# Kernel tuning notes

Measured on AMD Instinct MI355X. Metric: run time of the kernel, lower is better.

The kernel has to match this reference:

```python
import jax, jax.numpy as jnp
import numpy as np
from jax import lax

B, C, N, T = 8, 512, 256, 32  # batch, channels (c_in==c_out), nodes, timesteps


def setup_inputs() -> dict:
    key = jax.random.key(0)
    ks = jax.random.split(key, 5)
    x = jax.random.normal(ks[0], (B, C, N, T), dtype=jnp.float32)
    # 8 Line_Transforms: w1,w3,w5,w7 act on input x (gates i,f,o,g); w2,w4,w6,w8 act on h.
    # torch.rand init -> uniform [0,1). Weights (c_out,c_in), bias (c_in,1)==(C,1).
    Wx = jax.random.uniform(ks[1], (4, C, C), dtype=jnp.float32)
    bx = jax.random.uniform(ks[2], (4, C, 1), dtype=jnp.float32)
    Wh = jax.random.uniform(ks[3], (4, C, C), dtype=jnp.float32)
    bh = jax.random.uniform(ks[4], (4, C, 1), dtype=jnp.float32)
    return {"x": x, "Wx": Wx, "bx": bx, "Wh": Wh, "bh": bh}


def reference(x, Wx, bx, Wh, bh):
    b, f, n, t = x.shape
    c = Wx.shape[1]
    # Precompute all input-side gate projections for every timestep in one big GEMM.
    # xp: (T, 4, B, C, N); bias (4,C,1) broadcasts over batch and nodes.
    xp = jnp.einsum('gcf,bfnt->tgbcn', Wx, x) + bx[None, :, None]

    h0 = jnp.zeros((b, c, n), dtype=x.dtype)
    c0 = jnp.zeros((b, c, n), dtype=x.dtype)

    def step(carry, xp_t):
        h, cell = carry
        # hidden-side projections for all 4 gates at once: (4, B, C, N)
        hp = jnp.einsum('gcf,bfn->gbcn', Wh, h) + bh[:, None]
        z = xp_t + hp
        i = jax.nn.sigmoid(z[0])
        fg = jax.nn.sigmoid(z[1])
        o = jax.nn.sigmoid(z[2])
        g = jnp.tanh(z[3])
        new_c = fg * cell + i * g
        new_h = o * jnp.tanh(new_c)
        return (new_h, new_c), new_h

    _, hs = lax.scan(step, (h0, c0), xp)  # hs: (T, B, C, N)
    return jnp.moveaxis(hs, 0, -1)  # (B, C, N, T)
```

## Files before the change

### kernel.cpp

```cpp
#include <hip/hip_runtime.h>
#include <hip/hip_bf16.h>
#include <stdint.h>

typedef _Float16 f16x8 __attribute__((ext_vector_type(8)));
typedef float f32x16 __attribute__((ext_vector_type(16)));

#define MFMA __builtin_amdgcn_mfma_f32_32x32x16_f16

#define XP_OFF   0ull
#define HP_OFF   134217728ull
#define WT_OFF   142606336ull
#define BI_OFF   150994944ull
#define CS_OFF   151257088ull
#define HT_OFF   155451392ull

__device__ __forceinline__ void gload16(const void* g, void* s) {
    __builtin_amdgcn_global_load_lds((const __attribute__((address_space(1))) void*)g,
                                     (__attribute__((address_space(3))) void*)s, 16, 0, 0);
}

__global__ __launch_bounds__(256) void init_kernel(
    const float* __restrict__ Wx, const float* __restrict__ Wh,
    const float* __restrict__ bx, const float* __restrict__ bh, char* __restrict__ ws)
{
    f16x8* Wt = (f16x8*)(ws + WT_OFF);
    float* bi = (float*)(ws + BI_OFF);
    float4* cs = (float4*)(ws + CS_OFF);
    uint4* hp0 = (uint4*)(ws + HP_OFF);
    int tid = blockIdx.x * 256 + threadIdx.x;
    int stride = gridDim.x * 256;
    for (int i = tid; i < 262144; i += stride) {
        int l = i & 63, ks = (i >> 6) & 1, nt = (i >> 7) & 3, kk = (i >> 9) & 31, nblk = i >> 14;
        int n = nblk * 128 + nt * 32 + (l & 31);
        int k = kk * 32 + ks * 16 + 8 * (l >> 5);
        int c = n >> 2, g = n & 3;
        const float* src = (k < 512) ? (Wx + ((size_t)(g * 512 + c)) * 512 + k)
                                     : (Wh + ((size_t)(g * 512 + c)) * 512 + (k - 512));
        f16x8 hi, lo;
#pragma unroll
        for (int e = 0; e < 8; ++e) {
            float v = src[e];
            _Float16 h = (_Float16)v;
            hi[e] = h; lo[e] = (_Float16)(v - (float)h);
        }
        size_t base = (size_t)((i >> 6) * 2) * 64 + (i & 63);
        Wt[base] = hi;
        Wt[base + 64] = lo;
    }
    for (int i = tid; i < 65536; i += stride) {
        int r = i & 15, l = (i >> 4) & 63, nt = (i >> 10) & 3, nblk = i >> 12;
        int n = nblk * 128 + nt * 32 + (r & 3) + 8 * (r >> 2) + 4 * (l >> 5);
        int c = n >> 2, g = n & 3;
        bi[i] = bx[g * 512 + c] + bh[g * 512 + c];
    }
    for (int i = tid; i < 262144; i += stride) cs[i] = make_float4(0.f, 0.f, 0.f, 0.f);
    for (int i = tid; i < 262144; i += stride) hp0[i] = make_uint4(0u, 0u, 0u, 0u);
}

__global__ __launch_bounds__(256) void xpose_kernel(const float* __restrict__ x, f16x8* __restrict__ xp)
{
    __shared__ float tile[8448];
    int tid = threadIdx.x;
    int jblk = blockIdx.x, jt = blockIdx.y, fq = blockIdx.z;
    int jbase = jblk * 128 + jt * 32;
    for (int fg = 0; fg < 16; ++fg) {
        int fgg = fq * 16 + fg;
        {
            int jl = tid & 31, fo = tid >> 5;
            int j = jbase + jl, b = j >> 8, n = j & 255, f = fgg * 8 + fo;
            const float4* src = (const float4*)(x + (((size_t)(b * 512 + f)) * 256 + n) * 32);
            float* dst = &tile[(fo * 32 + jl) * 33];
#pragma unroll
            for (int i2 = 0; i2 < 8; ++i2) {
                float4 v = src[i2];
                dst[4 * i2 + 0] = v.x; dst[4 * i2 + 1] = v.y;
                dst[4 * i2 + 2] = v.z; dst[4 * i2 + 3] = v.w;
            }
        }
        __syncthreads();
        {
            int jl = tid & 31, tq = tid >> 5;
            int kk = fgg >> 2, ks = (fgg >> 1) & 1, hb = fgg & 1;
            int l = hb * 32 + jl;
#pragma unroll
            for (int ti = 0; ti < 4; ++ti) {
                int t = tq * 4 + ti;
                f16x8 hi, lo;
#pragma unroll
                for (int e = 0; e < 8; ++e) {
                    float v = tile[(e * 32 + jl) * 33 + t];
                    _Float16 h = (_Float16)v;
                    hi[e] = h; lo[e] = (_Float16)(v - (float)h);
                }
                size_t base = ((((size_t)t * 16 + jblk) * 16 + kk) * 4 + jt) * 4 + ks * 2;
                xp[(base + 0) * 64 + l] = hi;
                xp[(base + 1) * 64 + l] = lo;
            }
        }
        __syncthreads();
    }
}

__global__ __launch_bounds__(256, 1) void step_kernel(
    const f16x8* __restrict__ xp_t,
    const f16x8* __restrict__ hp_in,
    f16x8* __restrict__ hp_out,
    const f16x8* __restrict__ Wt,
    const float4* __restrict__ bi4,
    float4* __restrict__ cst4,
    _Float16* __restrict__ hsTt)
{
    __shared__ f16x8 actl[2][1024];
    const int tid = threadIdx.x;
    const int l = tid & 63;
    const int w = tid >> 6;
    const int wn = w >> 1, wj = w & 1;
    const int bid = blockIdx.x;
    const int idx = bid >> 3;
    const int nblk = ((bid & 7) << 1) | (idx & 1);
    const int jblk = idx >> 1;
    const int nt0 = wn * 2, jt0 = wj * 2;

    f32x16 acc00 = {0.f,0.f,0.f,0.f,0.f,0.f,0.f,0.f,0.f,0.f,0.f,0.f,0.f,0.f,0.f,0.f};
    f32x16 acc01 = acc00, acc10 = acc00, acc11 = acc00;
    f16x8 wtc0, wtc1, wtc2, wtc3, wtc4, wtc5, wtc6, wtc7;
    f16x8 wtn0, wtn1, wtn2, wtn3, wtn4, wtn5, wtn6, wtn7;

#define STAGE(bi_, kkv) do { \
    const f16x8* asrc = ((kkv) < 16) ? (xp_t + (size_t)(jblk * 16 + (kkv)) * 1024) \
                                     : (hp_in + (size_t)(jblk * 16 + ((kkv) - 16)) * 1024); \
    gload16(asrc + tid,       &actl[bi_][tid]); \
    gload16(asrc + tid + 256, &actl[bi_][tid + 256]); \
    gload16(asrc + tid + 512, &actl[bi_][tid + 512]); \
    gload16(asrc + tid + 768, &actl[bi_][tid + 768]); \
} while (0)

#define LOADW(P, kkv) do { \
    size_t wb = (size_t)((nblk * 32 + (kkv)) * 16 + nt0 * 4) * 64 + l; \
    P##0 = Wt[wb + 0 * 64]; P##1 = Wt[wb + 1 * 64]; P##2 = Wt[wb + 2 * 64]; P##3 = Wt[wb + 3 * 64]; \
    P##4 = Wt[wb + 4 * 64]; P##5 = Wt[wb + 5 * 64]; P##6 = Wt[wb + 6 * 64]; P##7 = Wt[wb + 7 * 64]; \
} while (0)

#define COMP_KS(bi_, whi0, wlo0, whi1, wlo1, ksv) do { \
    int ab = ((jt0 * 2 + (ksv)) * 2) * 64 + l; \
    f16x8 ahi0 = actl[bi_][ab], alo0 = actl[bi_][ab + 64]; \
    f16x8 ahi1 = actl[bi_][ab + 256], alo1 = actl[bi_][ab + 320]; \
    acc00 = MFMA(whi0, ahi0, acc00, 0, 0, 0); \
    acc00 = MFMA(wlo0, ahi0, acc00, 0, 0, 0); \
    acc00 = MFMA(whi0, alo0, acc00, 0, 0, 0); \
    acc01 = MFMA(whi0, ahi1, acc01, 0, 0, 0); \
    acc01 = MFMA(wlo0, ahi1, acc01, 0, 0, 0); \
    acc01 = MFMA(whi0, alo1, acc01, 0, 0, 0); \
    acc10 = MFMA(whi1, ahi0, acc10, 0, 0, 0); \
    acc10 = MFMA(wlo1, ahi0, acc10, 0, 0, 0); \
    acc10 = MFMA(whi1, alo0, acc10, 0, 0, 0); \
    acc11 = MFMA(whi1, ahi1, acc11, 0, 0, 0); \
    acc11 = MFMA(wlo1, ahi1, acc11, 0, 0, 0); \
    acc11 = MFMA(whi1, alo1, acc11, 0, 0, 0); \
} while (0)

#define COMPUTE(bi_, P) do { \
    COMP_KS(bi_, P##0, P##1, P##4, P##5, 0); \
    COMP_KS(bi_, P##2, P##3, P##6, P##7, 1); \
} while (0)

    STAGE(0, 0); LOADW(wtc, 0);
    __syncthreads();
    for (int kk2 = 0; kk2 < 16; ++kk2) {
        const int kkA = kk2 * 2;
        STAGE(1, kkA + 1); LOADW(wtn, kkA + 1);
        COMPUTE(0, wtc);
        __syncthreads();
        if (kk2 < 15) { STAGE(0, kkA + 2); LOADW(wtc, kkA + 2); }
        COMPUTE(1, wtn);
        __syncthreads();
    }

    const int p = l >> 5;
#define GATE(accV, q, bq, coldc, cnoutc, hqv) do { \
    float zi = accV[4 * (q) + 0] + bq.x; \
    float zf = accV[4 * (q) + 1] + bq.y; \
    float zo = accV[4 * (q) + 2] + bq.z; \
    float zg = accV[4 * (q) + 3] + bq.w; \
    float ig = 1.f / (1.f + expf(-zi)); \
    float fg = 1.f / (1.f + expf(-zf)); \
    float og = 1.f / (1.f + expf(-zo)); \
    float gg = tanhf(zg); \
    float cn = fg * coldc + ig * gg; \
    cnoutc = cn; \
    hqv = og * tanhf(cn); \
} while (0)

#define EPI(accV, ntl, jtl) do { \
    int nt = nt0 + (ntl), jt = jt0 + (jtl); \
    size_t bb = ((size_t)(nblk * 4 + nt) * 64 + l) * 4; \
    float4 bq0 = bi4[bb + 0], bq1 = bi4[bb + 1], bq2 = bi4[bb + 2], bq3 = bi4[bb + 3]; \
    size_t ci = (((size_t)(jblk * 16 + nblk) * 4 + jt) * 4 + nt) * 64 + l; \
    float4 cold = cst4[ci]; \
    float4 cnew; \
    float hq0, hq1, hq2, hq3; \
    GATE(accV, 0, bq0, cold.x, cnew.x, hq0); \
    GATE(accV, 1, bq1, cold.y, cnew.y, hq1); \
    GATE(accV, 2, bq2, cold.z, cnew.z, hq2); \
    GATE(accV, 3, bq3, cold.w, cnew.w, hq3); \
    cst4[ci] = cnew; \
    float hr0 = __shfl_xor(hq0, 32); \
    float hr1 = __shfl_xor(hq1, 32); \
    float hr2 = __shfl_xor(hq2, 32); \
    float hr3 = __shfl_xor(hq3, 32); \
    float e0 = p ? hr0 : hq0, e1 = p ? hq0 : hr0; \
    float e2 = p ? hr1 : hq1, e3 = p ? hq1 : hr1; \
    float e4 = p ? hr2 : hq2, e5 = p ? hq2 : hr2; \
    float e6 = p ? hr3 : hq3, e7 = p ? hq3 : hr3; \
    f16x8 hhi, hlo; \
    hhi[0] = (_Float16)e0; hhi[1] = (_Float16)e1; hhi[2] = (_Float16)e2; hhi[3] = (_Float16)e3; \
    hhi[4] = (_Float16)e4; hhi[5] = (_Float16)e5; hhi[6] = (_Float16)e6; hhi[7] = (_Float16)e7; \
    hlo[0] = (_Float16)(e0 - (float)hhi[0]); hlo[1] = (_Float16)(e1 - (float)hhi[1]); \
    hlo[2] = (_Float16)(e2 - (float)hhi[2]); hlo[3] = (_Float16)(e3 - (float)hhi[3]); \
    hlo[4] = (_Float16)(e4 - (float)hhi[4]); hlo[5] = (_Float16)(e5 - (float)hhi[5]); \
    hlo[6] = (_Float16)(e6 - (float)hhi[6]); hlo[7] = (_Float16)(e7 - (float)hhi[7]); \
    if (p == (nt & 1)) { \
        size_t hb = ((((size_t)(jblk * 16 + nblk) * 4 + jt) * 2 + (nt >> 1))) * 2; \
        hp_out[(hb + 0) * 64 + l] = hhi; \
        hp_out[(hb + 1) * 64 + l] = hlo; \
        int j = jblk * 128 + jt * 32 + (l & 31); \
        int c0 = nblk * 32 + nt * 8; \
        *(f16x8*)(hsTt + (size_t)j * 512 + c0) = hhi; \
    } \
} while (0)

    EPI(acc00, 0, 0);
    EPI(acc01, 0, 1);
    EPI(acc10, 1, 0);
    EPI(acc11, 1, 1);
}

__global__ __launch_bounds__(256) void oxpose_kernel(
    const _Float16* __restrict__ hsT, float* __restrict__ out)
{
    int tid = threadIdx.x;
    int bidx = blockIdx.x;
    int c = ((bidx & 1) << 8) + tid;
    int bn = bidx >> 1;
    int b = bn >> 8, n = bn & 255;
    float vals[32];
#pragma unroll
    for (int t = 0; t < 32; ++t)
        vals[t] = (float)hsT[((size_t)t * 2048 + bn) * 512 + c];
    float4* dst = (float4*)(out + (((size_t)(b * 512 + c)) * 256 + n) * 32);
#pragma unroll
    for (int i = 0; i < 8; ++i) {
        float4 v;
        v.x = vals[4 * i + 0]; v.y = vals[4 * i + 1];
        v.z = vals[4 * i + 2]; v.w = vals[4 * i + 3];
        dst[i] = v;
    }
}

extern "C" void kernel_launch(void* const* d_in, const int* in_sizes, int n_in,
                              void* d_out, int out_size, void* d_ws, size_t ws_size,
                              hipStream_t stream)
{
    const float* x  = (const float*)d_in[0];
    const float* Wx = (const float*)d_in[1];
    const float* bx = (const float*)d_in[2];
    const float* Wh = (const float*)d_in[3];
    const float* bh = (const float*)d_in[4];
    float* out = (float*)d_out;

    char* ws = (char*)d_ws;
    f16x8*  xp   = (f16x8*)(ws + XP_OFF);
    f16x8*  hp   = (f16x8*)(ws + HP_OFF);
    f16x8*  Wt   = (f16x8*)(ws + WT_OFF);
    float4* bi4  = (float4*)(ws + BI_OFF);
    float4* cst4 = (float4*)(ws + CS_OFF);
    _Float16* hsT = (_Float16*)(ws + HT_OFF);

    init_kernel<<<2048, 256, 0, stream>>>(Wx, Wh, bx, bh, ws);
    xpose_kernel<<<dim3(16, 4, 4), 256, 0, stream>>>(x, xp);
    for (int t = 0; t < 32; ++t) {
        step_kernel<<<256, 256, 0, stream>>>(
            xp + (size_t)t * 262144,
            hp + (size_t)(t & 1) * 262144,
            hp + (size_t)((t + 1) & 1) * 262144,
            Wt, bi4, cst4,
            hsT + (size_t)t * 2048 * 512);
    }
    oxpose_kernel<<<4096, 256, 0, stream>>>(hsT, out);
}
```

Measured before the change: 1.533 ms.

## Halve per-block step tile to double grid; flatten xpose loop across grid

The step kernel now gives each wave one n-tile instead of two, so each block computes half the output and the grid grows from 256 to 512 blocks. Launch bounds allow two blocks per CU, and per-wave weight registers and accumulators are halved. The xpose kernel drops its inner 16-iteration loop and launches 64 z-blocks instead of 4, which gives the transpose more parallelism. The cost is that each activation tile staged in LDS is reused by fewer MFMAs, so activation loads from global memory double.

```diff
diff --git a/kernel.cpp b/kernel.cpp
--- a/kernel.cpp
+++ b/kernel.cpp
@@ -61,47 +61,43 @@
 {
     __shared__ float tile[8448];
     int tid = threadIdx.x;
-    int jblk = blockIdx.x, jt = blockIdx.y, fq = blockIdx.z;
+    int jblk = blockIdx.x, jt = blockIdx.y, fgg = blockIdx.z;
     int jbase = jblk * 128 + jt * 32;
-    for (int fg = 0; fg < 16; ++fg) {
-        int fgg = fq * 16 + fg;
-        {
-            int jl = tid & 31, fo = tid >> 5;
-            int j = jbase + jl, b = j >> 8, n = j & 255, f = fgg * 8 + fo;
-            const float4* src = (const float4*)(x + (((size_t)(b * 512 + f)) * 256 + n) * 32);
-            float* dst = &tile[(fo * 32 + jl) * 33];
-#pragma unroll
-            for (int i2 = 0; i2 < 8; ++i2) {
-                float4 v = src[i2];
-                dst[4 * i2 + 0] = v.x; dst[4 * i2 + 1] = v.y;
-                dst[4 * i2 + 2] = v.z; dst[4 * i2 + 3] = v.w;
+    {
+        int jl = tid & 31, fo = tid >> 5;
+        int j = jbase + jl, b = j >> 8, n = j & 255, f = fgg * 8 + fo;
+        const float4* src = (const float4*)(x + (((size_t)(b * 512 + f)) * 256 + n) * 32);
+        float* dst = &tile[(fo * 32 + jl) * 33];
+#pragma unroll
+        for (int i2 = 0; i2 < 8; ++i2) {
+            float4 v = src[i2];
+            dst[4 * i2 + 0] = v.x; dst[4 * i2 + 1] = v.y;
+            dst[4 * i2 + 2] = v.z; dst[4 * i2 + 3] = v.w;
+        }
+    }
+    __syncthreads();
+    {
+        int jl = tid & 31, tq = tid >> 5;
+        int kk = fgg >> 2, ks = (fgg >> 1) & 1, hb = fgg & 1;
+        int l = hb * 32 + jl;
+#pragma unroll
+        for (int ti = 0; ti < 4; ++ti) {
+            int t = tq * 4 + ti;
+            f16x8 hi, lo;
+#pragma unroll
+            for (int e = 0; e < 8; ++e) {
+                float v = tile[(e * 32 + jl) * 33 + t];
+                _Float16 h = (_Float16)v;
+                hi[e] = h; lo[e] = (_Float16)(v - (float)h);
             }
+            size_t base = ((((size_t)t * 16 + jblk) * 16 + kk) * 4 + jt) * 4 + ks * 2;
+            xp[(base + 0) * 64 + l] = hi;
+            xp[(base + 1) * 64 + l] = lo;
         }
-        __syncthreads();
-        {
-            int jl = tid & 31, tq = tid >> 5;
-            int kk = fgg >> 2, ks = (fgg >> 1) & 1, hb = fgg & 1;
-            int l = hb * 32 + jl;
-#pragma unroll
-            for (int ti = 0; ti < 4; ++ti) {
-                int t = tq * 4 + ti;
-                f16x8 hi, lo;
-#pragma unroll
-                for (int e = 0; e < 8; ++e) {
-                    float v = tile[(e * 32 + jl) * 33 + t];
-                    _Float16 h = (_Float16)v;
-                    hi[e] = h; lo[e] = (_Float16)(v - (float)h);
-                }
-                size_t base = ((((size_t)t * 16 + jblk) * 16 + kk) * 4 + jt) * 4 + ks * 2;
-                xp[(base + 0) * 64 + l] = hi;
-                xp[(base + 1) * 64 + l] = lo;
-            }
-        }
-        __syncthreads();
-    }
-}
-
-__global__ __launch_bounds__(256, 1) void step_kernel(
+    }
+}
+
+__global__ __launch_bounds__(256, 2) void step_kernel(
     const f16x8* __restrict__ xp_t,
     const f16x8* __restrict__ hp_in,
     f16x8* __restrict__ hp_out,
@@ -117,14 +113,16 @@
     const int wn = w >> 1, wj = w & 1;
     const int bid = blockIdx.x;
     const int idx = bid >> 3;
-    const int nblk = ((bid & 7) << 1) | (idx & 1);
-    const int jblk = idx >> 1;
-    const int nt0 = wn * 2, jt0 = wj * 2;
-
-    f32x16 acc00 = {0.f,0.f,0.f,0.f,0.f,0.f,0.f,0.f,0.f,0.f,0.f,0.f,0.f,0.f,0.f,0.f};
-    f32x16 acc01 = acc00, acc10 = acc00, acc11 = acc00;
-    f16x8 wtc0, wtc1, wtc2, wtc3, wtc4, wtc5, wtc6, wtc7;
-    f16x8 wtn0, wtn1, wtn2, wtn3, wtn4, wtn5, wtn6, wtn7;
+    const int nblk4 = ((bid & 7) << 2) | (idx & 3);
+    const int jblk = idx >> 2;
+    const int nblk = nblk4 >> 1;
+    const int nt = ((nblk4 & 1) << 1) | wn;
+    const int jt0 = wj * 2;
+
+    f32x16 acc0 = {0.f,0.f,0.f,0.f,0.f,0.f,0.f,0.f,0.f,0.f,0.f,0.f,0.f,0.f,0.f,0.f};
+    f32x16 acc1 = acc0;
+    f16x8 wtc0, wtc1, wtc2, wtc3;
+    f16x8 wtn0, wtn1, wtn2, wtn3;
 
 #define STAGE(bi_, kkv) do { \
     const f16x8* asrc = ((kkv) < 16) ? (xp_t + (size_t)(jblk * 16 + (kkv)) * 1024) \
@@ -136,32 +134,26 @@
 } while (0)
 
 #define LOADW(P, kkv) do { \
-    size_t wb = (size_t)((nblk * 32 + (kkv)) * 16 + nt0 * 4) * 64 + l; \
-    P##0 = Wt[wb + 0 * 64]; P##1 = Wt[wb + 1 * 64]; P##2 = Wt[wb + 2 * 64]; P##3 = Wt[wb + 3 * 64]; \
-    P##4 = Wt[wb + 4 * 64]; P##5 = Wt[wb + 5 * 64]; P##6 = Wt[wb + 6 * 64]; P##7 = Wt[wb + 7 * 64]; \
-} while (0)
-
-#define COMP_KS(bi_, whi0, wlo0, whi1, wlo1, ksv) do { \
+    size_t wb = (size_t)((nblk * 32 + (kkv)) * 16 + nt * 4) * 64 + l; \
+    P##0 = Wt[wb + 0 * 64]; P##1 = Wt[wb + 1 * 64]; \
+    P##2 = Wt[wb + 2 * 64]; P##3 = Wt[wb + 3 * 64]; \
+} while (0)
+
+#define COMP_KS(bi_, whi, wlo, ksv) do { \
     int ab = ((jt0 * 2 + (ksv)) * 2) * 64 + l; \
     f16x8 ahi0 = actl[bi_][ab], alo0 = actl[bi_][ab + 64]; \
     f16x8 ahi1 = actl[bi_][ab + 256], alo1 = actl[bi_][ab + 320]; \
-    acc00 = MFMA(whi0, ahi0, acc00, 0, 0, 0); \
-    acc00 = MFMA(wlo0, ahi0, acc00, 0, 0, 0); \
-    acc00 = MFMA(whi0, alo0, acc00, 0, 0, 0); \
-    acc01 = MFMA(whi0, ahi1, acc01, 0, 0, 0); \
-    acc01 = MFMA(wlo0, ahi1, acc01, 0, 0, 0); \
-    acc01 = MFMA(whi0, alo1, acc01, 0, 0, 0); \
-    acc10 = MFMA(whi1, ahi0, acc10, 0, 0, 0); \
-    acc10 = MFMA(wlo1, ahi0, acc10, 0, 0, 0); \
-    acc10 = MFMA(whi1, alo0, acc10, 0, 0, 0); \
-    acc11 = MFMA(whi1, ahi1, acc11, 0, 0, 0); \
-    acc11 = MFMA(wlo1, ahi1, acc11, 0, 0, 0); \
-    acc11 = MFMA(whi1, alo1, acc11, 0, 0, 0); \
+    acc0 = MFMA(whi, ahi0, acc0, 0, 0, 0); \
+    acc0 = MFMA(wlo, ahi0, acc0, 0, 0, 0); \
+    acc0 = MFMA(whi, alo0, acc0, 0, 0, 0); \
+    acc1 = MFMA(whi, ahi1, acc1, 0, 0, 0); \
+    acc1 = MFMA(wlo, ahi1, acc1, 0, 0, 0); \
+    acc1 = MFMA(whi, alo1, acc1, 0, 0, 0); \
 } while (0)
 
 #define COMPUTE(bi_, P) do { \
-    COMP_KS(bi_, P##0, P##1, P##4, P##5, 0); \
-    COMP_KS(bi_, P##2, P##3, P##6, P##7, 1); \
+    COMP_KS(bi_, P##0, P##1, 0); \
+    COMP_KS(bi_, P##2, P##3, 1); \
 } while (0)
 
     STAGE(0, 0); LOADW(wtc, 0);
@@ -191,8 +183,8 @@
     hqv = og * tanhf(cn); \
 } while (0)
 
-#define EPI(accV, ntl, jtl) do { \
-    int nt = nt0 + (ntl), jt = jt0 + (jtl); \
+#define EPI(accV, jtl) do { \
+    int jt = jt0 + (jtl); \
     size_t bb = ((size_t)(nblk * 4 + nt) * 64 + l) * 4; \
     float4 bq0 = bi4[bb + 0], bq1 = bi4[bb + 1], bq2 = bi4[bb + 2], bq3 = bi4[bb + 3]; \
     size_t ci = (((size_t)(jblk * 16 + nblk) * 4 + jt) * 4 + nt) * 64 + l; \
@@ -229,10 +221,8 @@
     } \
 } while (0)
 
-    EPI(acc00, 0, 0);
-    EPI(acc01, 0, 1);
-    EPI(acc10, 1, 0);
-    EPI(acc11, 1, 1);
+    EPI(acc0, 0);
+    EPI(acc1, 1);
 }
 
 __global__ __launch_bounds__(256) void oxpose_kernel(
@@ -277,9 +267,9 @@
     _Float16* hsT = (_Float16*)(ws + HT_OFF);
 
     init_kernel<<<2048, 256, 0, stream>>>(Wx, Wh, bx, bh, ws);
-    xpose_kernel<<<dim3(16, 4, 4), 256, 0, stream>>>(x, xp);
+    xpose_kernel<<<dim3(16, 4, 64), 256, 0, stream>>>(x, xp);
     for (int t = 0; t < 32; ++t) {
-        step_kernel<<<256, 256, 0, stream>>>(
+        step_kernel<<<512, 256, 0, stream>>>(
             xp + (size_t)t * 262144,
             hp + (size_t)(t & 1) * 262144,
             hp + (size_t)((t + 1) & 1) * 262144,
```

After: 1.396 ms. -9.0%, faster.
